# Performance work log

Hardware: AMD Instinct MI355X
Metric: run time of the kernel (lower is better)

## Reference

```python
import jax, jax.numpy as jnp
import numpy as np

CHANNELS = 12
NUM_FREQ = 5
P = 1 + 2 * NUM_FREQ  # pos_embed_output_dim = 11
WORLD = (96, 96, 96)


def setup_inputs() -> dict:
    key = jax.random.key(0)
    k1, k2 = jax.random.split(key)
    xyz = jax.random.uniform(k1, (800000, 3), dtype=jnp.float32, minval=-1.0, maxval=1.0)
    # learned grid parameter [channels * P, *world_size] (torch inits zeros; use small randn for a non-trivial test)
    grid = jax.random.normal(k2, (CHANNELS * P,) + WORLD, dtype=jnp.float32) * 0.01
    xyz_min = jnp.array([-1.0, -1.0, -1.0], dtype=jnp.float32)
    xyz_max = jnp.array([1.0, 1.0, 1.0], dtype=jnp.float32)
    return {"xyz": xyz, "grid": grid, "xyz_min": xyz_min, "xyz_max": xyz_max}


def _trilinear_sample(g, coords):
    # g: [C, Dx, Dy, Dz]; coords: [N, 3] in [-1, 1] with
    # coords[:,0] -> last spatial dim Dz, coords[:,1] -> Dy, coords[:,2] -> Dx
    # (matches F.grid_sample 5D convention with align_corners=True)
    Dx, Dy, Dz = g.shape[1], g.shape[2], g.shape[3]

    def split(f, D):
        f = (f + 1.0) * 0.5 * (D - 1)  # align_corners=True mapping
        i0 = jnp.clip(jnp.floor(f).astype(jnp.int32), 0, D - 1)
        i1 = jnp.clip(i0 + 1, 0, D - 1)
        w = f - i0.astype(f.dtype)
        return i0, i1, w

    z0, z1, wz = split(coords[:, 0], Dz)
    y0, y1, wy = split(coords[:, 1], Dy)
    x0, x1, wx = split(coords[:, 2], Dx)

    def gather(ix, iy, iz):
        return g[:, ix, iy, iz]  # [C, N]

    c000 = gather(x0, y0, z0); c001 = gather(x0, y0, z1)
    c010 = gather(x0, y1, z0); c011 = gather(x0, y1, z1)
    c100 = gather(x1, y0, z0); c101 = gather(x1, y0, z1)
    c110 = gather(x1, y1, z0); c111 = gather(x1, y1, z1)

    c00 = c000 * (1 - wz) + c001 * wz
    c01 = c010 * (1 - wz) + c011 * wz
    c10 = c100 * (1 - wz) + c101 * wz
    c11 = c110 * (1 - wz) + c111 * wz
    c0 = c00 * (1 - wy) + c01 * wy
    c1 = c10 * (1 - wy) + c11 * wy
    return c0 * (1 - wx) + c1 * wx  # [C, N]


def reference(xyz, grid, xyz_min, xyz_max):
    shape = xyz.shape[:-1]
    pts = xyz.reshape(-1, 3)
    # normalize to [0,1], flip xyz -> zyx, map to [-1,1]
    ind_norm = ((pts - xyz_min) / (xyz_max - xyz_min))[:, ::-1] * 2.0 - 1.0  # [N, 3]

    freqs = 2.0 ** jnp.arange(NUM_FREQ, dtype=jnp.float32)
    comps = [ind_norm]
    for f in range(NUM_FREQ):
        comps.append(jnp.sin(freqs[f] * ind_norm))
        comps.append(jnp.cos(freqs[f] * ind_norm))
    comps = jnp.stack(comps, axis=0)  # [P, N, 3]

    grids = grid.reshape(P, CHANNELS, *WORLD)  # [P, C, Dx, Dy, Dz]
    sampled = jax.vmap(_trilinear_sample)(grids, comps)  # [P, C, N]
    out = jnp.mean(sampled, axis=0)  # [C, N]
    out = out.T.reshape(*shape, CHANNELS)  # [N, C]
    return out
```

## Files before the change

kernel.cpp:

```cpp
#include <hip/hip_runtime.h>
#include <hip/hip_fp16.h>
#include <cmath>

constexpr int D   = 96;
constexpr int C   = 12;
constexpr int P   = 11;
constexpr int NF  = 5;
constexpr int VOX = D * D * D;
constexpr int CELLS = 32 * 32 * 32;

__global__ __launch_bounds__(256) void transpose_fp16_kernel(
    const float* __restrict__ g, __half* __restrict__ gt) {
  constexpr int RPT = VOX / 4;
  int t = blockIdx.x * 256 + threadIdx.x;
  if (t >= P * RPT) return;
  int p = t / RPT;
  int r4 = (t - p * RPT) * 4;
  const float* src = g + (size_t)p * C * VOX + r4;

  float4 v[C];
#pragma unroll
  for (int c = 0; c < C; ++c)
    v[c] = *reinterpret_cast<const float4*>(src + (size_t)c * VOX);

  union { __half h[48]; uint4 u[6]; } pk;
#pragma unroll
  for (int j = 0; j < 4; ++j) {
#pragma unroll
    for (int c = 0; c < C; ++c) {
      float f = (j == 0) ? v[c].x : (j == 1) ? v[c].y : (j == 2) ? v[c].z : v[c].w;
      pk.h[j * C + c] = __float2half_rn(f);
    }
  }
  uint4* dst = reinterpret_cast<uint4*>(gt + ((size_t)p * VOX + r4) * C);
#pragma unroll
  for (int k = 0; k < 6; ++k) dst[k] = pk.u[k];
}

__device__ __forceinline__ unsigned spread5(unsigned v) {
  v &= 31u;
  v = (v | (v << 8)) & 0x100Fu;
  v = (v | (v << 4)) & 0x10C3u;
  v = (v | (v << 2)) & 0x1249u;
  return v;
}

__device__ __forceinline__ unsigned cell_of(const float* __restrict__ xyz, int n,
                                            const float* __restrict__ mn,
                                            const float* __restrict__ mx) {
  unsigned cc[3];
#pragma unroll
  for (int d = 0; d < 3; ++d) {
    float u = (xyz[3 * (size_t)n + d] - mn[d]) / (mx[d] - mn[d]);
    int c = (int)(u * 32.0f);
    c = c < 0 ? 0 : (c > 31 ? 31 : c);
    cc[d] = (unsigned)c;
  }
  return spread5(cc[0]) | (spread5(cc[1]) << 1) | (spread5(cc[2]) << 2);
}

__global__ __launch_bounds__(256) void count_kernel(
    const float* __restrict__ xyz, const float* __restrict__ mn,
    const float* __restrict__ mx, unsigned* __restrict__ counts, int N) {
  int n = blockIdx.x * 256 + threadIdx.x;
  if (n >= N) return;
  atomicAdd(&counts[cell_of(xyz, n, mn, mx)], 1u);
}

__global__ __launch_bounds__(1024) void scan_kernel(
    const unsigned* __restrict__ counts, unsigned* __restrict__ offsets) {
  __shared__ unsigned part[1024];
  int t = threadIdx.x;
  unsigned base = t * (CELLS / 1024);
  unsigned local[CELLS / 1024];
  unsigned s = 0;
#pragma unroll
  for (int i = 0; i < CELLS / 1024; ++i) { local[i] = s; s += counts[base + i]; }
  part[t] = s;
  __syncthreads();
  for (int off = 1; off < 1024; off <<= 1) {
    unsigned v = (t >= off) ? part[t - off] : 0u;
    __syncthreads();
    part[t] += v;
    __syncthreads();
  }
  unsigned prev = (t == 0) ? 0u : part[t - 1];
#pragma unroll
  for (int i = 0; i < CELLS / 1024; ++i) offsets[base + i] = prev + local[i];
}

__global__ __launch_bounds__(256) void scatter_kernel(
    const float* __restrict__ xyz, const float* __restrict__ mn,
    const float* __restrict__ mx, unsigned* __restrict__ offsets,
    float4* __restrict__ sorted, int N) {
  int n = blockIdx.x * 256 + threadIdx.x;
  if (n >= N) return;
  unsigned cell = cell_of(xyz, n, mn, mx);
  unsigned slot = atomicAdd(&offsets[cell], 1u);
  float4 rec;
  rec.x = xyz[3 * (size_t)n + 0];
  rec.y = xyz[3 * (size_t)n + 1];
  rec.z = xyz[3 * (size_t)n + 2];
  rec.w = __uint_as_float((unsigned)n);
  sorted[slot] = rec;
}

__global__ __launch_bounds__(256) void sample_sorted_kernel(
    const float4* __restrict__ pts, const __half* __restrict__ g,
    const float* __restrict__ xyz_min, const float* __restrict__ xyz_max,
    float* __restrict__ out, int N) {
  unsigned nwg = gridDim.x, bid = blockIdx.x;
  unsigned q = nwg / 8u, r = nwg % 8u;
  unsigned xcd = bid % 8u, j = bid / 8u;
  unsigned swz = (xcd < r ? xcd * (q + 1u) : r * (q + 1u) + (xcd - r) * q) + j;
  int n = swz * 256 + threadIdx.x;
  if (n >= N) return;

  float4 rec = pts[n];
  unsigned oidx = __float_as_uint(rec.w);
  float in[3] = {rec.x, rec.y, rec.z};
  float u[3];
#pragma unroll
  for (int d = 0; d < 3; ++d) {
    float mn = xyz_min[d], mx = xyz_max[d];
    u[d] = (in[d] - mn) * (2.0f / (mx - mn)) - 1.0f;
  }

  float acc[C];
#pragma unroll
  for (int c = 0; c < C; ++c) acc[c] = 0.0f;

  const ushort* gu = reinterpret_cast<const ushort*>(g);
  int p = 0;
  auto gather = [&](float ex, float ey, float ez) {
    float tz = (ez + 1.0f) * (0.5f * (D - 1));
    float ty = (ey + 1.0f) * (0.5f * (D - 1));
    float tx = (ex + 1.0f) * (0.5f * (D - 1));
    int z0 = (int)floorf(tz); z0 = z0 < 0 ? 0 : (z0 > D - 1 ? D - 1 : z0);
    int y0 = (int)floorf(ty); y0 = y0 < 0 ? 0 : (y0 > D - 1 ? D - 1 : y0);
    int x0 = (int)floorf(tx); x0 = x0 < 0 ? 0 : (x0 > D - 1 ? D - 1 : x0);
    int y1 = y0 + 1 > D - 1 ? D - 1 : y0 + 1;
    int x1 = x0 + 1 > D - 1 ? D - 1 : x0 + 1;
    float wz = tz - (float)z0, wy = ty - (float)y0, wx = tx - (float)x0;
    float wz0 = 1.0f - wz, wz1 = wz;
    float wy0 = 1.0f - wy, wy1 = wy;
    float wx0 = 1.0f - wx, wx1 = wx;

    size_t pbase = (size_t)p * VOX;
    const uint4* r00 = reinterpret_cast<const uint4*>(gu + (pbase + (size_t)((x0 * D + y0) * D + z0)) * C);
    const uint4* r01 = reinterpret_cast<const uint4*>(gu + (pbase + (size_t)((x0 * D + y1) * D + z0)) * C);
    const uint4* r10 = reinterpret_cast<const uint4*>(gu + (pbase + (size_t)((x1 * D + y0) * D + z0)) * C);
    const uint4* r11 = reinterpret_cast<const uint4*>(gu + (pbase + (size_t)((x1 * D + y1) * D + z0)) * C);

    uint4 a0 = r00[0], a1 = r00[1], a2 = r00[2];
    uint4 b0 = r01[0], b1 = r01[1], b2 = r01[2];
    uint4 c0 = r10[0], c1 = r10[1], c2 = r10[2];
    uint4 d0 = r11[0], d1 = r11[1], d2 = r11[2];

    auto acc2 = [&](unsigned lo, unsigned hi, float w0, float w1, int c) {
      __half2 hl = *reinterpret_cast<const __half2*>(&lo);
      __half2 hh = *reinterpret_cast<const __half2*>(&hi);
      float2 f0 = __half22float2(hl);
      float2 f1 = __half22float2(hh);
      acc[c]     = fmaf(w0, f0.x, fmaf(w1, f1.x, acc[c]));
      acc[c + 1] = fmaf(w0, f0.y, fmaf(w1, f1.y, acc[c + 1]));
    };
    auto region = [&](const uint4& q0, const uint4& q1, const uint4& q2, float wxy) {
      float w0 = wxy * wz0, w1 = wxy * wz1;
      acc2(q0.x, q1.z, w0, w1, 0);
      acc2(q0.y, q1.w, w0, w1, 2);
      acc2(q0.z, q2.x, w0, w1, 4);
      acc2(q0.w, q2.y, w0, w1, 6);
      acc2(q1.x, q2.z, w0, w1, 8);
      acc2(q1.y, q2.w, w0, w1, 10);
    };
    region(a0, a1, a2, wx0 * wy0);
    region(b0, b1, b2, wx0 * wy1);
    region(c0, c1, c2, wx1 * wy0);
    region(d0, d1, d2, wx1 * wy1);
    ++p;
  };

  gather(u[0], u[1], u[2]);
  float s[3], co[3];
#pragma unroll
  for (int d = 0; d < 3; ++d) { s[d] = sinf(u[d]); co[d] = cosf(u[d]); }
  for (int f = 0; f < NF; ++f) {
    gather(s[0], s[1], s[2]);
    gather(co[0], co[1], co[2]);
    if (f < NF - 1) {
#pragma unroll
      for (int d = 0; d < 3; ++d) {
        float ns = 2.0f * s[d] * co[d];
        float nc = 1.0f - 2.0f * s[d] * s[d];
        s[d] = ns; co[d] = nc;
      }
    }
  }

  constexpr float inv = 1.0f / (float)P;
  float4 r0, r1, r2;
  r0.x = acc[0] * inv;  r0.y = acc[1] * inv;  r0.z = acc[2] * inv;  r0.w = acc[3] * inv;
  r1.x = acc[4] * inv;  r1.y = acc[5] * inv;  r1.z = acc[6] * inv;  r1.w = acc[7] * inv;
  r2.x = acc[8] * inv;  r2.y = acc[9] * inv;  r2.z = acc[10] * inv; r2.w = acc[11] * inv;
  float4* o4 = reinterpret_cast<float4*>(out + (size_t)oidx * C);
  o4[0] = r0; o4[1] = r1; o4[2] = r2;
}

__global__ __launch_bounds__(256) void sample_fp16_kernel(
    const float* __restrict__ xyz, const __half* __restrict__ g,
    const float* __restrict__ xyz_min, const float* __restrict__ xyz_max,
    float* __restrict__ out, int N) {
  int n = blockIdx.x * 256 + threadIdx.x;
  if (n >= N) return;
  float u[3];
#pragma unroll
  for (int d = 0; d < 3; ++d) {
    float mn = xyz_min[d], mx = xyz_max[d];
    u[d] = (xyz[3 * (size_t)n + d] - mn) * (2.0f / (mx - mn)) - 1.0f;
  }
  float acc[C];
#pragma unroll
  for (int c = 0; c < C; ++c) acc[c] = 0.0f;
  const ushort* gu = reinterpret_cast<const ushort*>(g);
  int p = 0;
  auto gather = [&](float ex, float ey, float ez) {
    float tz = (ez + 1.0f) * (0.5f * (D - 1));
    float ty = (ey + 1.0f) * (0.5f * (D - 1));
    float tx = (ex + 1.0f) * (0.5f * (D - 1));
    int z0 = (int)floorf(tz); z0 = z0 < 0 ? 0 : (z0 > D - 1 ? D - 1 : z0);
    int y0 = (int)floorf(ty); y0 = y0 < 0 ? 0 : (y0 > D - 1 ? D - 1 : y0);
    int x0 = (int)floorf(tx); x0 = x0 < 0 ? 0 : (x0 > D - 1 ? D - 1 : x0);
    int y1 = y0 + 1 > D - 1 ? D - 1 : y0 + 1;
    int x1 = x0 + 1 > D - 1 ? D - 1 : x0 + 1;
    float wz = tz - (float)z0, wy = ty - (float)y0, wx = tx - (float)x0;
    float wz0 = 1.0f - wz, wz1 = wz;
    float wy0 = 1.0f - wy, wy1 = wy;
    float wx0 = 1.0f - wx, wx1 = wx;
    size_t pbase = (size_t)p * VOX;
    const uint4* r00 = reinterpret_cast<const uint4*>(gu + (pbase + (size_t)((x0 * D + y0) * D + z0)) * C);
    const uint4* r01 = reinterpret_cast<const uint4*>(gu + (pbase + (size_t)((x0 * D + y1) * D + z0)) * C);
    const uint4* r10 = reinterpret_cast<const uint4*>(gu + (pbase + (size_t)((x1 * D + y0) * D + z0)) * C);
    const uint4* r11 = reinterpret_cast<const uint4*>(gu + (pbase + (size_t)((x1 * D + y1) * D + z0)) * C);
    uint4 a0 = r00[0], a1 = r00[1], a2 = r00[2];
    uint4 b0 = r01[0], b1 = r01[1], b2 = r01[2];
    uint4 c0 = r10[0], c1 = r10[1], c2 = r10[2];
    uint4 d0 = r11[0], d1 = r11[1], d2 = r11[2];
    auto acc2 = [&](unsigned lo, unsigned hi, float w0, float w1, int c) {
      __half2 hl = *reinterpret_cast<const __half2*>(&lo);
      __half2 hh = *reinterpret_cast<const __half2*>(&hi);
      float2 f0 = __half22float2(hl);
      float2 f1 = __half22float2(hh);
      acc[c]     = fmaf(w0, f0.x, fmaf(w1, f1.x, acc[c]));
      acc[c + 1] = fmaf(w0, f0.y, fmaf(w1, f1.y, acc[c + 1]));
    };
    auto region = [&](const uint4& q0, const uint4& q1, const uint4& q2, float wxy) {
      float w0 = wxy * wz0, w1 = wxy * wz1;
      acc2(q0.x, q1.z, w0, w1, 0);
      acc2(q0.y, q1.w, w0, w1, 2);
      acc2(q0.z, q2.x, w0, w1, 4);
      acc2(q0.w, q2.y, w0, w1, 6);
      acc2(q1.x, q2.z, w0, w1, 8);
      acc2(q1.y, q2.w, w0, w1, 10);
    };
    region(a0, a1, a2, wx0 * wy0);
    region(b0, b1, b2, wx0 * wy1);
    region(c0, c1, c2, wx1 * wy0);
    region(d0, d1, d2, wx1 * wy1);
    ++p;
  };
  gather(u[0], u[1], u[2]);
  float s[3], co[3];
#pragma unroll
  for (int d = 0; d < 3; ++d) { s[d] = sinf(u[d]); co[d] = cosf(u[d]); }
  for (int f = 0; f < NF; ++f) {
    gather(s[0], s[1], s[2]);
    gather(co[0], co[1], co[2]);
    if (f < NF - 1) {
#pragma unroll
      for (int d = 0; d < 3; ++d) {
        float ns = 2.0f * s[d] * co[d];
        float nc = 1.0f - 2.0f * s[d] * s[d];
        s[d] = ns; co[d] = nc;
      }
    }
  }
  constexpr float inv = 1.0f / (float)P;
  float4 r0, r1, r2;
  r0.x = acc[0] * inv;  r0.y = acc[1] * inv;  r0.z = acc[2] * inv;  r0.w = acc[3] * inv;
  r1.x = acc[4] * inv;  r1.y = acc[5] * inv;  r1.z = acc[6] * inv;  r1.w = acc[7] * inv;
  r2.x = acc[8] * inv;  r2.y = acc[9] * inv;  r2.z = acc[10] * inv; r2.w = acc[11] * inv;
  float4* o4 = reinterpret_cast<float4*>(out + (size_t)n * C);
  o4[0] = r0; o4[1] = r1; o4[2] = r2;
}

__global__ __launch_bounds__(256) void sample_naive_kernel(
    const float* __restrict__ xyz, const float* __restrict__ g,
    const float* __restrict__ xyz_min, const float* __restrict__ xyz_max,
    float* __restrict__ out, int N) {
  int n = blockIdx.x * 256 + threadIdx.x;
  if (n >= N) return;
  float u[3];
#pragma unroll
  for (int d = 0; d < 3; ++d) {
    float mn = xyz_min[d], mx = xyz_max[d];
    u[d] = (xyz[3 * (size_t)n + d] - mn) * (2.0f / (mx - mn)) - 1.0f;
  }
  float acc[C];
#pragma unroll
  for (int c = 0; c < C; ++c) acc[c] = 0.0f;
  int p = 0;
  auto gather = [&](float ex, float ey, float ez) {
    float e[3] = {ez, ey, ex};
    int i0[3], i1[3]; float w[3];
#pragma unroll
    for (int d = 0; d < 3; ++d) {
      float t = (e[d] + 1.0f) * (0.5f * (D - 1));
      int a = (int)floorf(t);
      a = a < 0 ? 0 : (a > D - 1 ? D - 1 : a);
      int b = a + 1 > D - 1 ? D - 1 : a + 1;
      i0[d] = a; i1[d] = b; w[d] = t - (float)a;
    }
    const float* gp = g + (size_t)p * C * VOX;
    auto corner = [&](int iz, int iy, int ix, float wgt) {
      int o = (ix * D + iy) * D + iz;
#pragma unroll
      for (int c = 0; c < C; ++c) acc[c] += wgt * gp[(size_t)c * VOX + o];
    };
    corner(i0[0], i0[1], i0[2], (1 - w[0]) * (1 - w[1]) * (1 - w[2]));
    corner(i1[0], i0[1], i0[2], w[0] * (1 - w[1]) * (1 - w[2]));
    corner(i0[0], i1[1], i0[2], (1 - w[0]) * w[1] * (1 - w[2]));
    corner(i1[0], i1[1], i0[2], w[0] * w[1] * (1 - w[2]));
    corner(i0[0], i0[1], i1[2], (1 - w[0]) * (1 - w[1]) * w[2]);
    corner(i1[0], i0[1], i1[2], w[0] * (1 - w[1]) * w[2]);
    corner(i0[0], i1[1], i1[2], (1 - w[0]) * w[1] * w[2]);
    corner(i1[0], i1[1], i1[2], w[0] * w[1] * w[2]);
    ++p;
  };
  gather(u[0], u[1], u[2]);
  float s[3], co[3];
#pragma unroll
  for (int d = 0; d < 3; ++d) { s[d] = sinf(u[d]); co[d] = cosf(u[d]); }
  for (int f = 0; f < NF; ++f) {
    gather(s[0], s[1], s[2]);
    gather(co[0], co[1], co[2]);
    if (f < NF - 1) {
#pragma unroll
      for (int d = 0; d < 3; ++d) {
        float ns = 2.0f * s[d] * co[d];
        float nc = 1.0f - 2.0f * s[d] * s[d];
        s[d] = ns; co[d] = nc;
      }
    }
  }
  constexpr float inv = 1.0f / (float)P;
#pragma unroll
  for (int c = 0; c < C; ++c) out[(size_t)n * C + c] = acc[c] * inv;
}

extern "C" void kernel_launch(void* const* d_in, const int* in_sizes, int n_in,
                              void* d_out, int out_size, void* d_ws, size_t ws_size,
                              hipStream_t stream) {
  const float* xyz = (const float*)d_in[0];
  const float* grid = (const float*)d_in[1];
  const float* mn = (const float*)d_in[2];
  const float* mx = (const float*)d_in[3];
  float* out = (float*)d_out;
  int N = in_sizes[0] / 3;

  size_t gt_bytes = (size_t)P * VOX * C * sizeof(__half);
  size_t sorted_bytes = (size_t)N * sizeof(float4);
  size_t cnt_bytes = (size_t)CELLS * sizeof(unsigned);
  size_t need_sorted = sorted_bytes + gt_bytes + 2 * cnt_bytes + 1024;
  size_t need_plain  = gt_bytes + 256;

  int sblocks = (N + 255) / 256;
  int tblocks = (P * (VOX / 4) + 255) / 256;

  if (ws_size >= need_sorted) {
    char* w = (char*)d_ws;
    float4*   sorted  = (float4*)w;                  w += sorted_bytes;
    __half*   gt      = (__half*)w;                  w += gt_bytes;
    unsigned* counts  = (unsigned*)w;                w += cnt_bytes;
    unsigned* offsets = (unsigned*)w;

    transpose_fp16_kernel<<<tblocks, 256, 0, stream>>>(grid, gt);
    hipMemsetAsync(counts, 0, cnt_bytes, stream);
    count_kernel<<<sblocks, 256, 0, stream>>>(xyz, mn, mx, counts, N);
    scan_kernel<<<1, 1024, 0, stream>>>(counts, offsets);
    scatter_kernel<<<sblocks, 256, 0, stream>>>(xyz, mn, mx, offsets, sorted, N);
    sample_sorted_kernel<<<sblocks, 256, 0, stream>>>(sorted, gt, mn, mx, out, N);
  } else if (ws_size >= need_plain) {
    __half* gt = (__half*)d_ws;
    transpose_fp16_kernel<<<tblocks, 256, 0, stream>>>(grid, gt);
    sample_fp16_kernel<<<sblocks, 256, 0, stream>>>(xyz, gt, mn, mx, out, N);
  } else {
    sample_naive_kernel<<<sblocks, 256, 0, stream>>>(xyz, grid, mn, mx, out, N);
  }
}
```

Before: 577.3 us.

## Split sampling into low/high-frequency passes with separate periodic spatial sort

Sampling is split into two kernels. One handles the identity plane and the first two frequency planes, using points sorted by a Morton cell of the normalized coordinate. The other handles the three highest frequency planes, using a second ordering keyed on the fractional part of u·4/π. Because those high-frequency sin/cos embeddings are periodic in u, points that share a phase cell should touch nearby grid voxels, which should improve cache reuse for gathers that were scattered before. The cost is a second counting sort, a second sorted buffer, an extra kernel launch, and a read-modify-write of the output in the high pass.

```diff
diff --git a/kernel.cpp b/kernel.cpp
--- a/kernel.cpp
+++ b/kernel.cpp
@@ -5,7 +5,6 @@
 constexpr int D   = 96;
 constexpr int C   = 12;
 constexpr int P   = 11;
-constexpr int NF  = 5;
 constexpr int VOX = D * D * D;
 constexpr int CELLS = 32 * 32 * 32;
 
@@ -45,30 +44,55 @@
   return v;
 }
 
-__device__ __forceinline__ unsigned cell_of(const float* __restrict__ xyz, int n,
-                                            const float* __restrict__ mn,
-                                            const float* __restrict__ mx) {
+__device__ __forceinline__ unsigned cellA_of(const float u[3]) {
   unsigned cc[3];
 #pragma unroll
   for (int d = 0; d < 3; ++d) {
-    float u = (xyz[3 * (size_t)n + d] - mn[d]) / (mx[d] - mn[d]);
-    int c = (int)(u * 32.0f);
+    int c = (int)((u[d] + 1.0f) * 16.0f);
     c = c < 0 ? 0 : (c > 31 ? 31 : c);
     cc[d] = (unsigned)c;
   }
   return spread5(cc[0]) | (spread5(cc[1]) << 1) | (spread5(cc[2]) << 2);
 }
 
-__global__ __launch_bounds__(256) void count_kernel(
+__device__ __forceinline__ unsigned cellB_of(const float u[3]) {
+  unsigned cc[3];
+#pragma unroll
+  for (int d = 0; d < 3; ++d) {
+    float v = u[d] * 1.27323954f;
+    float f = v - floorf(v);
+    int c = (int)(f * 32.0f);
+    c = c < 0 ? 0 : (c > 31 ? 31 : c);
+    cc[d] = (unsigned)c;
+  }
+  return spread5(cc[0]) | (spread5(cc[1]) << 1) | (spread5(cc[2]) << 2);
+}
+
+__device__ __forceinline__ void norm_u(const float* __restrict__ xyz, int n,
+                                       const float* __restrict__ mn,
+                                       const float* __restrict__ mx, float u[3]) {
+#pragma unroll
+  for (int d = 0; d < 3; ++d)
+    u[d] = (xyz[3 * (size_t)n + d] - mn[d]) * (2.0f / (mx[d] - mn[d])) - 1.0f;
+}
+
+__global__ __launch_bounds__(256) void count_both_kernel(
     const float* __restrict__ xyz, const float* __restrict__ mn,
-    const float* __restrict__ mx, unsigned* __restrict__ counts, int N) {
+    const float* __restrict__ mx, unsigned* __restrict__ cntA,
+    unsigned* __restrict__ cntB, int N, int doB) {
   int n = blockIdx.x * 256 + threadIdx.x;
   if (n >= N) return;
-  atomicAdd(&counts[cell_of(xyz, n, mn, mx)], 1u);
-}
-
-__global__ __launch_bounds__(1024) void scan_kernel(
-    const unsigned* __restrict__ counts, unsigned* __restrict__ offsets) {
+  float u[3];
+  norm_u(xyz, n, mn, mx, u);
+  atomicAdd(&cntA[cellA_of(u)], 1u);
+  if (doB) atomicAdd(&cntB[cellB_of(u)], 1u);
+}
+
+__global__ __launch_bounds__(1024) void scan2_kernel(
+    const unsigned* __restrict__ cntA, unsigned* __restrict__ offA,
+    const unsigned* __restrict__ cntB, unsigned* __restrict__ offB) {
+  const unsigned* counts = (blockIdx.x == 0) ? cntA : cntB;
+  unsigned* offsets = (blockIdx.x == 0) ? offA : offB;
   __shared__ unsigned part[1024];
   int t = threadIdx.x;
   unsigned base = t * (CELLS / 1024);
@@ -89,42 +113,43 @@
   for (int i = 0; i < CELLS / 1024; ++i) offsets[base + i] = prev + local[i];
 }
 
-__global__ __launch_bounds__(256) void scatter_kernel(
+__global__ __launch_bounds__(256) void scatter_both_kernel(
     const float* __restrict__ xyz, const float* __restrict__ mn,
-    const float* __restrict__ mx, unsigned* __restrict__ offsets,
-    float4* __restrict__ sorted, int N) {
+    const float* __restrict__ mx, unsigned* __restrict__ offA,
+    unsigned* __restrict__ offB, float4* __restrict__ sortedA,
+    float4* __restrict__ sortedB, int N, int doB) {
   int n = blockIdx.x * 256 + threadIdx.x;
   if (n >= N) return;
-  unsigned cell = cell_of(xyz, n, mn, mx);
-  unsigned slot = atomicAdd(&offsets[cell], 1u);
+  float u[3];
+  norm_u(xyz, n, mn, mx, u);
   float4 rec;
-  rec.x = xyz[3 * (size_t)n + 0];
-  rec.y = xyz[3 * (size_t)n + 1];
-  rec.z = xyz[3 * (size_t)n + 2];
+  rec.x = u[0]; rec.y = u[1]; rec.z = u[2];
   rec.w = __uint_as_float((unsigned)n);
-  sorted[slot] = rec;
-}
-
-__global__ __launch_bounds__(256) void sample_sorted_kernel(
-    const float4* __restrict__ pts, const __half* __restrict__ g,
-    const float* __restrict__ xyz_min, const float* __restrict__ xyz_max,
-    float* __restrict__ out, int N) {
+  unsigned sa = atomicAdd(&offA[cellA_of(u)], 1u);
+  sortedA[sa] = rec;
+  if (doB) {
+    unsigned sb = atomicAdd(&offB[cellB_of(u)], 1u);
+    sortedB[sb] = rec;
+  }
+}
+
+__device__ __forceinline__ int swz_point(int N) {
   unsigned nwg = gridDim.x, bid = blockIdx.x;
   unsigned q = nwg / 8u, r = nwg % 8u;
   unsigned xcd = bid % 8u, j = bid / 8u;
   unsigned swz = (xcd < r ? xcd * (q + 1u) : r * (q + 1u) + (xcd - r) * q) + j;
-  int n = swz * 256 + threadIdx.x;
+  return (int)(swz * 256u + threadIdx.x);
+}
+
+__global__ __launch_bounds__(256) void sample_lo_kernel(
+    const float4* __restrict__ pts, const __half* __restrict__ g,
+    float* __restrict__ out, int N) {
+  int n = swz_point(N);
   if (n >= N) return;
 
   float4 rec = pts[n];
   unsigned oidx = __float_as_uint(rec.w);
-  float in[3] = {rec.x, rec.y, rec.z};
-  float u[3];
-#pragma unroll
-  for (int d = 0; d < 3; ++d) {
-    float mn = xyz_min[d], mx = xyz_max[d];
-    u[d] = (in[d] - mn) * (2.0f / (mx - mn)) - 1.0f;
-  }
+  float u[3] = {rec.x, rec.y, rec.z};
 
   float acc[C];
 #pragma unroll
@@ -185,10 +210,10 @@
   float s[3], co[3];
 #pragma unroll
   for (int d = 0; d < 3; ++d) { s[d] = sinf(u[d]); co[d] = cosf(u[d]); }
-  for (int f = 0; f < NF; ++f) {
+  for (int f = 0; f < 2; ++f) {
     gather(s[0], s[1], s[2]);
     gather(co[0], co[1], co[2]);
-    if (f < NF - 1) {
+    if (f < 1) {
 #pragma unroll
       for (int d = 0; d < 3; ++d) {
         float ns = 2.0f * s[d] * co[d];
@@ -204,6 +229,99 @@
   r1.x = acc[4] * inv;  r1.y = acc[5] * inv;  r1.z = acc[6] * inv;  r1.w = acc[7] * inv;
   r2.x = acc[8] * inv;  r2.y = acc[9] * inv;  r2.z = acc[10] * inv; r2.w = acc[11] * inv;
   float4* o4 = reinterpret_cast<float4*>(out + (size_t)oidx * C);
+  o4[0] = r0; o4[1] = r1; o4[2] = r2;
+}
+
+__global__ __launch_bounds__(256) void sample_hi_kernel(
+    const float4* __restrict__ pts, const __half* __restrict__ g,
+    float* __restrict__ out, int N) {
+  int n = swz_point(N);
+  if (n >= N) return;
+
+  float4 rec = pts[n];
+  unsigned oidx = __float_as_uint(rec.w);
+  float u[3] = {rec.x, rec.y, rec.z};
+
+  float acc[C];
+#pragma unroll
+  for (int c = 0; c < C; ++c) acc[c] = 0.0f;
+
+  const ushort* gu = reinterpret_cast<const ushort*>(g);
+  int p = 5;
+  auto gather = [&](float ex, float ey, float ez) {
+    float tz = (ez + 1.0f) * (0.5f * (D - 1));
+    float ty = (ey + 1.0f) * (0.5f * (D - 1));
+    float tx = (ex + 1.0f) * (0.5f * (D - 1));
+    int z0 = (int)floorf(tz); z0 = z0 < 0 ? 0 : (z0 > D - 1 ? D - 1 : z0);
+    int y0 = (int)floorf(ty); y0 = y0 < 0 ? 0 : (y0 > D - 1 ? D - 1 : y0);
+    int x0 = (int)floorf(tx); x0 = x0 < 0 ? 0 : (x0 > D - 1 ? D - 1 : x0);
+    int y1 = y0 + 1 > D - 1 ? D - 1 : y0 + 1;
+    int x1 = x0 + 1 > D - 1 ? D - 1 : x0 + 1;
+    float wz = tz - (float)z0, wy = ty - (float)y0, wx = tx - (float)x0;
+    float wz0 = 1.0f - wz, wz1 = wz;
+    float wy0 = 1.0f - wy, wy1 = wy;
+    float wx0 = 1.0f - wx, wx1 = wx;
+
+    size_t pbase = (size_t)p * VOX;
+    const uint4* r00 = reinterpret_cast<const uint4*>(gu + (pbase + (size_t)((x0 * D + y0) * D + z0)) * C);
+    const uint4* r01 = reinterpret_cast<const uint4*>(gu + (pbase + (size_t)((x0 * D + y1) * D + z0)) * C);
+    const uint4* r10 = reinterpret_cast<const uint4*>(gu + (pbase + (size_t)((x1 * D + y0) * D + z0)) * C);
+    const uint4* r11 = reinterpret_cast<const uint4*>(gu + (pbase + (size_t)((x1 * D + y1) * D + z0)) * C);
+
+    uint4 a0 = r00[0], a1 = r00[1], a2 = r00[2];
+    uint4 b0 = r01[0], b1 = r01[1], b2 = r01[2];
+    uint4 c0 = r10[0], c1 = r10[1], c2 = r10[2];
+    uint4 d0 = r11[0], d1 = r11[1], d2 = r11[2];
+
+    auto acc2 = [&](unsigned lo, unsigned hi, float w0, float w1, int c) {
+      __half2 hl = *reinterpret_cast<const __half2*>(&lo);
+      __half2 hh = *reinterpret_cast<const __half2*>(&hi);
+      float2 f0 = __half22float2(hl);
+      float2 f1 = __half22float2(hh);
+      acc[c]     = fmaf(w0, f0.x, fmaf(w1, f1.x, acc[c]));
+      acc[c + 1] = fmaf(w0, f0.y, fmaf(w1, f1.y, acc[c + 1]));
+    };
+    auto region = [&](const uint4& q0, const uint4& q1, const uint4& q2, float wxy) {
+      float w0 = wxy * wz0, w1 = wxy * wz1;
+      acc2(q0.x, q1.z, w0, w1, 0);
+      acc2(q0.y, q1.w, w0, w1, 2);
+      acc2(q0.z, q2.x, w0, w1, 4);
+      acc2(q0.w, q2.y, w0, w1, 6);
+      acc2(q1.x, q2.z, w0, w1, 8);
+      acc2(q1.y, q2.w, w0, w1, 10);
+    };
+    region(a0, a1, a2, wx0 * wy0);
+    region(b0, b1, b2, wx0 * wy1);
+    region(c0, c1, c2, wx1 * wy0);
+    region(d0, d1, d2, wx1 * wy1);
+    ++p;
+  };
+
+  float s[3], co[3];
+#pragma unroll
+  for (int d = 0; d < 3; ++d) {
+    float a = 4.0f * u[d];
+    s[d] = sinf(a); co[d] = cosf(a);
+  }
+  for (int f = 0; f < 3; ++f) {
+    gather(s[0], s[1], s[2]);
+    gather(co[0], co[1], co[2]);
+    if (f < 2) {
+#pragma unroll
+      for (int d = 0; d < 3; ++d) {
+        float ns = 2.0f * s[d] * co[d];
+        float nc = 1.0f - 2.0f * s[d] * s[d];
+        s[d] = ns; co[d] = nc;
+      }
+    }
+  }
+
+  constexpr float inv = 1.0f / (float)P;
+  float4* o4 = reinterpret_cast<float4*>(out + (size_t)oidx * C);
+  float4 r0 = o4[0], r1 = o4[1], r2 = o4[2];
+  r0.x += acc[0] * inv;  r0.y += acc[1] * inv;  r0.z += acc[2] * inv;  r0.w += acc[3] * inv;
+  r1.x += acc[4] * inv;  r1.y += acc[5] * inv;  r1.z += acc[6] * inv;  r1.w += acc[7] * inv;
+  r2.x += acc[8] * inv;  r2.y += acc[9] * inv;  r2.z += acc[10] * inv; r2.w += acc[11] * inv;
   o4[0] = r0; o4[1] = r1; o4[2] = r2;
 }
 
@@ -273,10 +391,10 @@
   float s[3], co[3];
 #pragma unroll
   for (int d = 0; d < 3; ++d) { s[d] = sinf(u[d]); co[d] = cosf(u[d]); }
-  for (int f = 0; f < NF; ++f) {
+  for (int f = 0; f < 5; ++f) {
     gather(s[0], s[1], s[2]);
     gather(co[0], co[1], co[2]);
-    if (f < NF - 1) {
+    if (f < 4) {
 #pragma unroll
       for (int d = 0; d < 3; ++d) {
         float ns = 2.0f * s[d] * co[d];
@@ -341,10 +459,10 @@
   float s[3], co[3];
 #pragma unroll
   for (int d = 0; d < 3; ++d) { s[d] = sinf(u[d]); co[d] = cosf(u[d]); }
-  for (int f = 0; f < NF; ++f) {
+  for (int f = 0; f < 5; ++f) {
     gather(s[0], s[1], s[2]);
     gather(co[0], co[1], co[2]);
-    if (f < NF - 1) {
+    if (f < 4) {
 #pragma unroll
       for (int d = 0; d < 3; ++d) {
         float ns = 2.0f * s[d] * co[d];
@@ -371,26 +489,38 @@
   size_t gt_bytes = (size_t)P * VOX * C * sizeof(__half);
   size_t sorted_bytes = (size_t)N * sizeof(float4);
   size_t cnt_bytes = (size_t)CELLS * sizeof(unsigned);
-  size_t need_sorted = sorted_bytes + gt_bytes + 2 * cnt_bytes + 1024;
-  size_t need_plain  = gt_bytes + 256;
+
+  size_t need_full = 2 * sorted_bytes + gt_bytes + 4 * cnt_bytes + 1024;
+  size_t need_one  = sorted_bytes + gt_bytes + 2 * cnt_bytes + 1024;
+  size_t need_min  = gt_bytes + 256;
 
   int sblocks = (N + 255) / 256;
   int tblocks = (P * (VOX / 4) + 255) / 256;
 
-  if (ws_size >= need_sorted) {
+  if (ws_size >= need_one) {
+    int doB = (ws_size >= need_full) ? 1 : 0;
     char* w = (char*)d_ws;
-    float4*   sorted  = (float4*)w;                  w += sorted_bytes;
-    __half*   gt      = (__half*)w;                  w += gt_bytes;
-    unsigned* counts  = (unsigned*)w;                w += cnt_bytes;
-    unsigned* offsets = (unsigned*)w;
+    float4* sortedA = (float4*)w;                     w += sorted_bytes;
+    float4* sortedB = doB ? (float4*)w : sortedA;     if (doB) w += sorted_bytes;
+    __half* gt      = (__half*)w;                     w += gt_bytes;
+    unsigned* cntA  = (unsigned*)w;                   w += cnt_bytes;
+    unsigned* offA  = (unsigned*)w;                   w += cnt_bytes;
+    unsigned* cntB  = cntA;
+    unsigned* offB  = offA;
+    if (doB) {
+      cntB = (unsigned*)w;  w += cnt_bytes;
+      offB = (unsigned*)w;
+    }
 
     transpose_fp16_kernel<<<tblocks, 256, 0, stream>>>(grid, gt);
-    hipMemsetAsync(counts, 0, cnt_bytes, stream);
-    count_kernel<<<sblocks, 256, 0, stream>>>(xyz, mn, mx, counts, N);
-    scan_kernel<<<1, 1024, 0, stream>>>(counts, offsets);
-    scatter_kernel<<<sblocks, 256, 0, stream>>>(xyz, mn, mx, offsets, sorted, N);
-    sample_sorted_kernel<<<sblocks, 256, 0, stream>>>(sorted, gt, mn, mx, out, N);
-  } else if (ws_size >= need_plain) {
+    hipMemsetAsync(cntA, 0, (doB ? 4 : 2) * cnt_bytes, stream);
+    count_both_kernel<<<sblocks, 256, 0, stream>>>(xyz, mn, mx, cntA, cntB, N, doB);
+    scan2_kernel<<<doB ? 2 : 1, 1024, 0, stream>>>(cntA, offA, cntB, offB);
+    scatter_both_kernel<<<sblocks, 256, 0, stream>>>(xyz, mn, mx, offA, offB,
+                                                     sortedA, sortedB, N, doB);
+    sample_lo_kernel<<<sblocks, 256, 0, stream>>>(sortedA, gt, out, N);
+    sample_hi_kernel<<<sblocks, 256, 0, stream>>>(sortedB, gt, out, N);
+  } else if (ws_size >= need_min) {
     __half* gt = (__half*)d_ws;
     transpose_fp16_kernel<<<tblocks, 256, 0, stream>>>(grid, gt);
     sample_fp16_kernel<<<sblocks, 256, 0, stream>>>(xyz, gt, mn, mx, out, N);
```

Result: slower. 697.9 us (+20.9%).

## Fuse transpose with count, pre-normalize sorted points, sample two points per thread

Applied to the files above, without the earlier changes.

Merges the grid fp16 transpose and the cell-count pass into one kernel, which removes a launch and a separate pass over xyz. The scatter now stores already-normalized coordinates, so the sampler no longer reads min/max. The sampler processes two consecutive sorted points per thread, issuing 24 uint4 loads before consuming any, to raise memory-level parallelism. This roughly doubles register pressure and halves the thread count, which may reduce occupancy.

```diff
diff --git a/kernel.cpp b/kernel.cpp
--- a/kernel.cpp
+++ b/kernel.cpp
@@ -5,37 +5,8 @@
 constexpr int D   = 96;
 constexpr int C   = 12;
 constexpr int P   = 11;
-constexpr int NF  = 5;
 constexpr int VOX = D * D * D;
 constexpr int CELLS = 32 * 32 * 32;
-
-__global__ __launch_bounds__(256) void transpose_fp16_kernel(
-    const float* __restrict__ g, __half* __restrict__ gt) {
-  constexpr int RPT = VOX / 4;
-  int t = blockIdx.x * 256 + threadIdx.x;
-  if (t >= P * RPT) return;
-  int p = t / RPT;
-  int r4 = (t - p * RPT) * 4;
-  const float* src = g + (size_t)p * C * VOX + r4;
-
-  float4 v[C];
-#pragma unroll
-  for (int c = 0; c < C; ++c)
-    v[c] = *reinterpret_cast<const float4*>(src + (size_t)c * VOX);
-
-  union { __half h[48]; uint4 u[6]; } pk;
-#pragma unroll
-  for (int j = 0; j < 4; ++j) {
-#pragma unroll
-    for (int c = 0; c < C; ++c) {
-      float f = (j == 0) ? v[c].x : (j == 1) ? v[c].y : (j == 2) ? v[c].z : v[c].w;
-      pk.h[j * C + c] = __float2half_rn(f);
-    }
-  }
-  uint4* dst = reinterpret_cast<uint4*>(gt + ((size_t)p * VOX + r4) * C);
-#pragma unroll
-  for (int k = 0; k < 6; ++k) dst[k] = pk.u[k];
-}
 
 __device__ __forceinline__ unsigned spread5(unsigned v) {
   v &= 31u;
@@ -45,26 +16,59 @@
   return v;
 }
 
-__device__ __forceinline__ unsigned cell_of(const float* __restrict__ xyz, int n,
-                                            const float* __restrict__ mn,
-                                            const float* __restrict__ mx) {
+__device__ __forceinline__ unsigned cell_of_u(const float u[3]) {
   unsigned cc[3];
 #pragma unroll
   for (int d = 0; d < 3; ++d) {
-    float u = (xyz[3 * (size_t)n + d] - mn[d]) / (mx[d] - mn[d]);
-    int c = (int)(u * 32.0f);
+    int c = (int)((u[d] + 1.0f) * 16.0f);
     c = c < 0 ? 0 : (c > 31 ? 31 : c);
     cc[d] = (unsigned)c;
   }
   return spread5(cc[0]) | (spread5(cc[1]) << 1) | (spread5(cc[2]) << 2);
 }
 
-__global__ __launch_bounds__(256) void count_kernel(
+__device__ __forceinline__ void norm_u(const float* __restrict__ xyz, int n,
+                                       const float* __restrict__ mn,
+                                       const float* __restrict__ mx, float u[3]) {
+#pragma unroll
+  for (int d = 0; d < 3; ++d)
+    u[d] = (xyz[3 * (size_t)n + d] - mn[d]) * (2.0f / (mx[d] - mn[d])) - 1.0f;
+}
+
+__global__ __launch_bounds__(256) void transpose_count_kernel(
+    const float* __restrict__ g, __half* __restrict__ gt,
     const float* __restrict__ xyz, const float* __restrict__ mn,
     const float* __restrict__ mx, unsigned* __restrict__ counts, int N) {
-  int n = blockIdx.x * 256 + threadIdx.x;
-  if (n >= N) return;
-  atomicAdd(&counts[cell_of(xyz, n, mn, mx)], 1u);
+  constexpr int RPT = VOX / 4;
+  int t = blockIdx.x * 256 + threadIdx.x;
+
+  if (t < P * RPT) {
+    int p = t / RPT;
+    int r4 = (t - p * RPT) * 4;
+    const float* src = g + (size_t)p * C * VOX + r4;
+    float4 v[C];
+#pragma unroll
+    for (int c = 0; c < C; ++c)
+      v[c] = *reinterpret_cast<const float4*>(src + (size_t)c * VOX);
+    union { __half h[48]; uint4 u[6]; } pk;
+#pragma unroll
+    for (int j = 0; j < 4; ++j) {
+#pragma unroll
+      for (int c = 0; c < C; ++c) {
+        float f = (j == 0) ? v[c].x : (j == 1) ? v[c].y : (j == 2) ? v[c].z : v[c].w;
+        pk.h[j * C + c] = __float2half_rn(f);
+      }
+    }
+    uint4* dst = reinterpret_cast<uint4*>(gt + ((size_t)p * VOX + r4) * C);
+#pragma unroll
+    for (int k = 0; k < 6; ++k) dst[k] = pk.u[k];
+  }
+
+  if (t < N) {
+    float u[3];
+    norm_u(xyz, t, mn, mx, u);
+    atomicAdd(&counts[cell_of_u(u)], 1u);
+  }
 }
 
 __global__ __launch_bounds__(1024) void scan_kernel(
@@ -95,44 +99,45 @@
     float4* __restrict__ sorted, int N) {
   int n = blockIdx.x * 256 + threadIdx.x;
   if (n >= N) return;
-  unsigned cell = cell_of(xyz, n, mn, mx);
-  unsigned slot = atomicAdd(&offsets[cell], 1u);
+  float u[3];
+  norm_u(xyz, n, mn, mx, u);
+  unsigned slot = atomicAdd(&offsets[cell_of_u(u)], 1u);
   float4 rec;
-  rec.x = xyz[3 * (size_t)n + 0];
-  rec.y = xyz[3 * (size_t)n + 1];
-  rec.z = xyz[3 * (size_t)n + 2];
+  rec.x = u[0]; rec.y = u[1]; rec.z = u[2];
   rec.w = __uint_as_float((unsigned)n);
   sorted[slot] = rec;
 }
 
-__global__ __launch_bounds__(256) void sample_sorted_kernel(
+__global__ __launch_bounds__(256) void sample_pair_kernel(
     const float4* __restrict__ pts, const __half* __restrict__ g,
-    const float* __restrict__ xyz_min, const float* __restrict__ xyz_max,
     float* __restrict__ out, int N) {
   unsigned nwg = gridDim.x, bid = blockIdx.x;
   unsigned q = nwg / 8u, r = nwg % 8u;
   unsigned xcd = bid % 8u, j = bid / 8u;
   unsigned swz = (xcd < r ? xcd * (q + 1u) : r * (q + 1u) + (xcd - r) * q) + j;
-  int n = swz * 256 + threadIdx.x;
-  if (n >= N) return;
-
-  float4 rec = pts[n];
-  unsigned oidx = __float_as_uint(rec.w);
-  float in[3] = {rec.x, rec.y, rec.z};
-  float u[3];
-#pragma unroll
-  for (int d = 0; d < 3; ++d) {
-    float mn = xyz_min[d], mx = xyz_max[d];
-    u[d] = (in[d] - mn) * (2.0f / (mx - mn)) - 1.0f;
-  }
-
-  float acc[C];
-#pragma unroll
-  for (int c = 0; c < C; ++c) acc[c] = 0.0f;
+  int n0 = (int)(swz * 512u + threadIdx.x * 2u);
+  int n1 = n0 + 1;
+  if (n0 >= N) return;
+  bool hasB = (n1 < N);
+
+  float4 recA = pts[n0];
+  float4 recB = hasB ? pts[n1] : recA;
+  unsigned oiA = __float_as_uint(recA.w);
+  unsigned oiB = __float_as_uint(recB.w);
+  float uA[3] = {recA.x, recA.y, recA.z};
+  float uB[3] = {recB.x, recB.y, recB.z};
+
+  float accA[C], accB[C];
+#pragma unroll
+  for (int c = 0; c < C; ++c) { accA[c] = 0.0f; accB[c] = 0.0f; }
 
   const ushort* gu = reinterpret_cast<const ushort*>(g);
   int p = 0;
-  auto gather = [&](float ex, float ey, float ez) {
+
+  auto setup = [&](float ex, float ey, float ez, size_t pbase,
+                   const uint4*& r00, const uint4*& r01,
+                   const uint4*& r10, const uint4*& r11,
+                   float& wz0, float& wz1, float w4[4]) {
     float tz = (ez + 1.0f) * (0.5f * (D - 1));
     float ty = (ey + 1.0f) * (0.5f * (D - 1));
     float tx = (ex + 1.0f) * (0.5f * (D - 1));
@@ -142,22 +147,20 @@
     int y1 = y0 + 1 > D - 1 ? D - 1 : y0 + 1;
     int x1 = x0 + 1 > D - 1 ? D - 1 : x0 + 1;
     float wz = tz - (float)z0, wy = ty - (float)y0, wx = tx - (float)x0;
-    float wz0 = 1.0f - wz, wz1 = wz;
+    wz0 = 1.0f - wz; wz1 = wz;
     float wy0 = 1.0f - wy, wy1 = wy;
     float wx0 = 1.0f - wx, wx1 = wx;
-
-    size_t pbase = (size_t)p * VOX;
-    const uint4* r00 = reinterpret_cast<const uint4*>(gu + (pbase + (size_t)((x0 * D + y0) * D + z0)) * C);
-    const uint4* r01 = reinterpret_cast<const uint4*>(gu + (pbase + (size_t)((x0 * D + y1) * D + z0)) * C);
-    const uint4* r10 = reinterpret_cast<const uint4*>(gu + (pbase + (size_t)((x1 * D + y0) * D + z0)) * C);
-    const uint4* r11 = reinterpret_cast<const uint4*>(gu + (pbase + (size_t)((x1 * D + y1) * D + z0)) * C);
-
-    uint4 a0 = r00[0], a1 = r00[1], a2 = r00[2];
-    uint4 b0 = r01[0], b1 = r01[1], b2 = r01[2];
-    uint4 c0 = r10[0], c1 = r10[1], c2 = r10[2];
-    uint4 d0 = r11[0], d1 = r11[1], d2 = r11[2];
-
-    auto acc2 = [&](unsigned lo, unsigned hi, float w0, float w1, int c) {
+    w4[0] = wx0 * wy0; w4[1] = wx0 * wy1; w4[2] = wx1 * wy0; w4[3] = wx1 * wy1;
+    r00 = reinterpret_cast<const uint4*>(gu + (pbase + (size_t)((x0 * D + y0) * D + z0)) * C);
+    r01 = reinterpret_cast<const uint4*>(gu + (pbase + (size_t)((x0 * D + y1) * D + z0)) * C);
+    r10 = reinterpret_cast<const uint4*>(gu + (pbase + (size_t)((x1 * D + y0) * D + z0)) * C);
+    r11 = reinterpret_cast<const uint4*>(gu + (pbase + (size_t)((x1 * D + y1) * D + z0)) * C);
+  };
+
+  auto consume = [&](float* acc, const uint4& q0, const uint4& q1, const uint4& q2,
+                     float wxy, float wz0, float wz1) {
+    float w0 = wxy * wz0, w1 = wxy * wz1;
+    auto acc2 = [&](unsigned lo, unsigned hi, int c) {
       __half2 hl = *reinterpret_cast<const __half2*>(&lo);
       __half2 hh = *reinterpret_cast<const __half2*>(&hi);
       float2 f0 = __half22float2(hl);
@@ -165,46 +168,83 @@
       acc[c]     = fmaf(w0, f0.x, fmaf(w1, f1.x, acc[c]));
       acc[c + 1] = fmaf(w0, f0.y, fmaf(w1, f1.y, acc[c + 1]));
     };
-    auto region = [&](const uint4& q0, const uint4& q1, const uint4& q2, float wxy) {
-      float w0 = wxy * wz0, w1 = wxy * wz1;
-      acc2(q0.x, q1.z, w0, w1, 0);
-      acc2(q0.y, q1.w, w0, w1, 2);
-      acc2(q0.z, q2.x, w0, w1, 4);
-      acc2(q0.w, q2.y, w0, w1, 6);
-      acc2(q1.x, q2.z, w0, w1, 8);
-      acc2(q1.y, q2.w, w0, w1, 10);
-    };
-    region(a0, a1, a2, wx0 * wy0);
-    region(b0, b1, b2, wx0 * wy1);
-    region(c0, c1, c2, wx1 * wy0);
-    region(d0, d1, d2, wx1 * wy1);
+    acc2(q0.x, q1.z, 0);
+    acc2(q0.y, q1.w, 2);
+    acc2(q0.z, q2.x, 4);
+    acc2(q0.w, q2.y, 6);
+    acc2(q1.x, q2.z, 8);
+    acc2(q1.y, q2.w, 10);
+  };
+
+  auto gather2 = [&](float exA, float eyA, float ezA,
+                     float exB, float eyB, float ezB) {
+    size_t pbase = (size_t)p * VOX;
+    const uint4 *a00, *a01, *a10, *a11, *b00, *b01, *b10, *b11;
+    float az0, az1, bz0, bz1, wA[4], wB[4];
+    setup(exA, eyA, ezA, pbase, a00, a01, a10, a11, az0, az1, wA);
+    setup(exB, eyB, ezB, pbase, b00, b01, b10, b11, bz0, bz1, wB);
+
+    uint4 A0 = a00[0], A1 = a00[1], A2 = a00[2];
+    uint4 A3 = a01[0], A4 = a01[1], A5 = a01[2];
+    uint4 A6 = a10[0], A7 = a10[1], A8 = a10[2];
+    uint4 A9 = a11[0], Aa = a11[1], Ab = a11[2];
+    uint4 B0 = b00[0], B1 = b00[1], B2 = b00[2];
+    uint4 B3 = b01[0], B4 = b01[1], B5 = b01[2];
+    uint4 B6 = b10[0], B7 = b10[1], B8 = b10[2];
+    uint4 B9 = b11[0], Ba = b11[1], Bb = b11[2];
+
+    consume(accA, A0, A1, A2, wA[0], az0, az1);
+    consume(accA, A3, A4, A5, wA[1], az0, az1);
+    consume(accA, A6, A7, A8, wA[2], az0, az1);
+    consume(accA, A9, Aa, Ab, wA[3], az0, az1);
+    consume(accB, B0, B1, B2, wB[0], bz0, bz1);
+    consume(accB, B3, B4, B5, wB[1], bz0, bz1);
+    consume(accB, B6, B7, B8, wB[2], bz0, bz1);
+    consume(accB, B9, Ba, Bb, wB[3], bz0, bz1);
     ++p;
   };
 
-  gather(u[0], u[1], u[2]);
-  float s[3], co[3];
-#pragma unroll
-  for (int d = 0; d < 3; ++d) { s[d] = sinf(u[d]); co[d] = cosf(u[d]); }
-  for (int f = 0; f < NF; ++f) {
-    gather(s[0], s[1], s[2]);
-    gather(co[0], co[1], co[2]);
-    if (f < NF - 1) {
+  gather2(uA[0], uA[1], uA[2], uB[0], uB[1], uB[2]);
+
+  float sA[3], cA[3], sB[3], cB[3];
+#pragma unroll
+  for (int d = 0; d < 3; ++d) {
+    sA[d] = sinf(uA[d]); cA[d] = cosf(uA[d]);
+    sB[d] = sinf(uB[d]); cB[d] = cosf(uB[d]);
+  }
+  for (int f = 0; f < 5; ++f) {
+    gather2(sA[0], sA[1], sA[2], sB[0], sB[1], sB[2]);
+    gather2(cA[0], cA[1], cA[2], cB[0], cB[1], cB[2]);
+    if (f < 4) {
 #pragma unroll
       for (int d = 0; d < 3; ++d) {
-        float ns = 2.0f * s[d] * co[d];
-        float nc = 1.0f - 2.0f * s[d] * s[d];
-        s[d] = ns; co[d] = nc;
+        float nsA = 2.0f * sA[d] * cA[d];
+        float ncA = 1.0f - 2.0f * sA[d] * sA[d];
+        sA[d] = nsA; cA[d] = ncA;
+        float nsB = 2.0f * sB[d] * cB[d];
+        float ncB = 1.0f - 2.0f * sB[d] * sB[d];
+        sB[d] = nsB; cB[d] = ncB;
       }
     }
   }
 
   constexpr float inv = 1.0f / (float)P;
-  float4 r0, r1, r2;
-  r0.x = acc[0] * inv;  r0.y = acc[1] * inv;  r0.z = acc[2] * inv;  r0.w = acc[3] * inv;
-  r1.x = acc[4] * inv;  r1.y = acc[5] * inv;  r1.z = acc[6] * inv;  r1.w = acc[7] * inv;
-  r2.x = acc[8] * inv;  r2.y = acc[9] * inv;  r2.z = acc[10] * inv; r2.w = acc[11] * inv;
-  float4* o4 = reinterpret_cast<float4*>(out + (size_t)oidx * C);
-  o4[0] = r0; o4[1] = r1; o4[2] = r2;
+  {
+    float4 r0, r1, r2;
+    r0.x = accA[0] * inv;  r0.y = accA[1] * inv;  r0.z = accA[2] * inv;  r0.w = accA[3] * inv;
+    r1.x = accA[4] * inv;  r1.y = accA[5] * inv;  r1.z = accA[6] * inv;  r1.w = accA[7] * inv;
+    r2.x = accA[8] * inv;  r2.y = accA[9] * inv;  r2.z = accA[10] * inv; r2.w = accA[11] * inv;
+    float4* o4 = reinterpret_cast<float4*>(out + (size_t)oiA * C);
+    o4[0] = r0; o4[1] = r1; o4[2] = r2;
+  }
+  if (hasB) {
+    float4 r0, r1, r2;
+    r0.x = accB[0] * inv;  r0.y = accB[1] * inv;  r0.z = accB[2] * inv;  r0.w = accB[3] * inv;
+    r1.x = accB[4] * inv;  r1.y = accB[5] * inv;  r1.z = accB[6] * inv;  r1.w = accB[7] * inv;
+    r2.x = accB[8] * inv;  r2.y = accB[9] * inv;  r2.z = accB[10] * inv; r2.w = accB[11] * inv;
+    float4* o4 = reinterpret_cast<float4*>(out + (size_t)oiB * C);
+    o4[0] = r0; o4[1] = r1; o4[2] = r2;
+  }
 }
 
 __global__ __launch_bounds__(256) void sample_fp16_kernel(
@@ -273,10 +313,10 @@
   float s[3], co[3];
 #pragma unroll
   for (int d = 0; d < 3; ++d) { s[d] = sinf(u[d]); co[d] = cosf(u[d]); }
-  for (int f = 0; f < NF; ++f) {
+  for (int f = 0; f < 5; ++f) {
     gather(s[0], s[1], s[2]);
     gather(co[0], co[1], co[2]);
-    if (f < NF - 1) {
+    if (f < 4) {
 #pragma unroll
       for (int d = 0; d < 3; ++d) {
         float ns = 2.0f * s[d] * co[d];
@@ -341,10 +381,10 @@
   float s[3], co[3];
 #pragma unroll
   for (int d = 0; d < 3; ++d) { s[d] = sinf(u[d]); co[d] = cosf(u[d]); }
-  for (int f = 0; f < NF; ++f) {
+  for (int f = 0; f < 5; ++f) {
     gather(s[0], s[1], s[2]);
     gather(co[0], co[1], co[2]);
-    if (f < NF - 1) {
+    if (f < 4) {
 #pragma unroll
       for (int d = 0; d < 3; ++d) {
         float ns = 2.0f * s[d] * co[d];
@@ -371,28 +411,31 @@
   size_t gt_bytes = (size_t)P * VOX * C * sizeof(__half);
   size_t sorted_bytes = (size_t)N * sizeof(float4);
   size_t cnt_bytes = (size_t)CELLS * sizeof(unsigned);
+
   size_t need_sorted = sorted_bytes + gt_bytes + 2 * cnt_bytes + 1024;
-  size_t need_plain  = gt_bytes + 256;
+  size_t need_min = gt_bytes + 256;
 
   int sblocks = (N + 255) / 256;
   int tblocks = (P * (VOX / 4) + 255) / 256;
 
   if (ws_size >= need_sorted) {
     char* w = (char*)d_ws;
-    float4*   sorted  = (float4*)w;                  w += sorted_bytes;
-    __half*   gt      = (__half*)w;                  w += gt_bytes;
-    unsigned* counts  = (unsigned*)w;                w += cnt_bytes;
+    float4*   sorted  = (float4*)w;   w += sorted_bytes;
+    __half*   gt      = (__half*)w;   w += gt_bytes;
+    unsigned* counts  = (unsigned*)w; w += cnt_bytes;
     unsigned* offsets = (unsigned*)w;
 
-    transpose_fp16_kernel<<<tblocks, 256, 0, stream>>>(grid, gt);
     hipMemsetAsync(counts, 0, cnt_bytes, stream);
-    count_kernel<<<sblocks, 256, 0, stream>>>(xyz, mn, mx, counts, N);
+    transpose_count_kernel<<<tblocks, 256, 0, stream>>>(grid, gt, xyz, mn, mx,
+                                                        counts, N);
     scan_kernel<<<1, 1024, 0, stream>>>(counts, offsets);
     scatter_kernel<<<sblocks, 256, 0, stream>>>(xyz, mn, mx, offsets, sorted, N);
-    sample_sorted_kernel<<<sblocks, 256, 0, stream>>>(sorted, gt, mn, mx, out, N);
-  } else if (ws_size >= need_plain) {
+    int pblocks = (N + 511) / 512;
+    sample_pair_kernel<<<pblocks, 256, 0, stream>>>(sorted, gt, out, N);
+  } else if (ws_size >= need_min) {
     __half* gt = (__half*)d_ws;
-    transpose_fp16_kernel<<<tblocks, 256, 0, stream>>>(grid, gt);
+    transpose_count_kernel<<<tblocks, 256, 0, stream>>>(grid, gt, xyz, mn, mx,
+                                                        nullptr, 0);
     sample_fp16_kernel<<<sblocks, 256, 0, stream>>>(xyz, gt, mn, mx, out, N);
   } else {
     sample_naive_kernel<<<sblocks, 256, 0, stream>>>(xyz, grid, mn, mx, out, N);
```

Result: no change. 586.7 us, median of 2 (+1.6%).
